# Performance work log

Measured on AMD Instinct MI355X. Metric: run time of the kernel, lower is better.

Reference implementation:

```python
import jax, jax.numpy as jnp
import numpy as np

EPSILON = 1e-06
MAXIMUM_AREA_RATIO = 0.3
GRID_HEIGHT = 160.0
CUBE = (25.0, 25.0, 32.0)
FEAT_SCALE = 1.0
GRID_SCALE = 1.0
CRANGE = (-1.0, 0.95)


def setup_inputs() -> dict:
    key = jax.random.key(0)
    k1, k2, k3, k4, k5 = jax.random.split(key, 5)
    B, C, H, W = 2, 256, 96, 320
    L, Wg = 128, 128
    n_layers = int(GRID_HEIGHT // CUBE[2])  # 5
    return {
        "feature": jax.random.normal(k1, (B, C, H, W), dtype=jnp.float32),
        "calib": jax.random.normal(k2, (B, 3, 4), dtype=jnp.float32),
        "grid": jax.random.normal(k3, (L, Wg, 3), dtype=jnp.float32),
        "Wc": jax.random.normal(k4, (C, C * n_layers), dtype=jnp.float32) * 0.02,
        "bc": jax.random.normal(k5, (C,), dtype=jnp.float32) * 0.02,
    }


def _cube_corners(cube):
    l, w, h = cube
    x = np.array([-l / 2, l / 2, l / 2, -l / 2, -l / 2, l / 2, l / 2, -l / 2])
    y = np.array([-w / 2, -w / 2, w / 2, w / 2, -w / 2, -w / 2, w / 2, w / 2])
    z = np.array([0, 0, 0, 0, h, h, h, h])
    return jnp.asarray(np.stack([x, y, z], axis=-1), dtype=jnp.float32)  # (8,3)


def _grid_sample_zeros(img, grd):
    # img: [B,C,H,W]; grd: [B,Hg,Wg,2] normalized coords in [-1,1]
    # bilinear, zero padding, align_corners=False (torch default)
    B, C, H, W = img.shape
    x = ((grd[..., 0] + 1.0) * W - 1.0) * 0.5
    y = ((grd[..., 1] + 1.0) * H - 1.0) * 0.5
    x0f = jnp.floor(x)
    y0f = jnp.floor(y)
    x0 = x0f.astype(jnp.int32)
    y0 = y0f.astype(jnp.int32)
    img_flat = img.reshape(B, C, H * W)

    def gather(xi, yi):
        valid = (xi >= 0) & (xi < W) & (yi >= 0) & (yi < H)
        xc = jnp.clip(xi, 0, W - 1)
        yc = jnp.clip(yi, 0, H - 1)
        idx = (yc * W + xc).reshape(B, 1, -1)
        v = jnp.take_along_axis(img_flat, idx, axis=2)
        v = v.reshape((B, C) + grd.shape[1:-1])
        return v * valid[:, None].astype(img.dtype)

    wx1 = x - x0f
    wx0 = 1.0 - wx1
    wy1 = y - y0f
    wy0 = 1.0 - wy1
    out = (gather(x0, y0) * (wx0 * wy0)[:, None]
           + gather(x0 + 1, y0) * (wx1 * wy0)[:, None]
           + gather(x0, y0 + 1) * (wx0 * wy1)[:, None]
           + gather(x0 + 1, y0 + 1) * (wx1 * wy1)[:, None])
    return out


def reference(feature, calib, grid, Wc, bc):
    B, C, H, W = feature.shape
    L, Wg, _ = grid.shape
    dtype = feature.dtype

    # z-layer offsets: (n_layers, 3) with offset only in z
    z_off = jnp.arange(0.0, GRID_HEIGHT, CUBE[2], dtype=dtype)  # (5,)
    n_layers = z_off.shape[0]
    z_corners = jnp.stack([jnp.zeros_like(z_off), jnp.zeros_like(z_off), z_off], axis=-1)
    offset = _cube_corners(CUBE)  # (8,3)

    # corners3d: (n_layers, L, Wg, 8, 3)
    corners = grid[None] + z_corners[:, None, None, :]  # (n,L,Wg,3)
    corners3d = (corners[:, :, :, None, :] + offset[None, None, None]) / GRID_SCALE

    # project with calib (B,3,4): homogeneous matmul then perspective divide
    hom = jnp.concatenate([corners3d, jnp.ones_like(corners3d[..., :1])], axis=-1)  # (n,L,Wg,8,4)
    pts = jnp.einsum('bij,nlwkj->bnlwki', calib, hom)  # (B,n,L,Wg,8,3)
    img_xy = pts[..., :2] / jnp.maximum(pts[..., 2:3], EPSILON)

    img_size = jnp.array([W, H], dtype=dtype) / FEAT_SCALE
    norm = jnp.clip(2.0 * img_xy / img_size - 1.0, CRANGE[0], CRANGE[1])  # (B,n,L,Wg,8,2)

    box_corners = jnp.concatenate([
        jnp.min(norm[..., 0], axis=-1, keepdims=True),
        jnp.min(norm[..., 1], axis=-1, keepdims=True),
        jnp.max(norm[..., 0], axis=-1, keepdims=True),
        jnp.max(norm[..., 1], axis=-1, keepdims=True),
    ], axis=-1)  # (B,n,L,Wg,4)
    box_corners = box_corners.reshape(B, n_layers, L * Wg, 4)

    area = ((box_corners[..., 2:] - box_corners[..., :2]).prod(axis=-1) * (H * W) + EPSILON)
    area = area[:, None]  # (B,1,n,LWg)
    visible = ((area > EPSILON) & (area < H * W * MAXIMUM_AREA_RATIO)).astype(dtype)

    integral = jnp.cumsum(jnp.cumsum(feature, axis=-1), axis=-2)

    lt = _grid_sample_zeros(integral, box_corners[..., [0, 1]])
    rb = _grid_sample_zeros(integral, box_corners[..., [2, 3]])
    rt = _grid_sample_zeros(integral, box_corners[..., [2, 1]])
    lb = _grid_sample_zeros(integral, box_corners[..., [0, 3]])

    vox = (lt + rb - rt - lb) / area * visible  # (B,C,n,LWg)
    # permute(0,3,1,2) -> (B, LWg, C, n); flatten to (B*LWg, C*n)
    vox = jnp.transpose(vox, (0, 3, 1, 2)).reshape(B * L * Wg, C * n_layers)

    ortho = vox @ Wc.T + bc  # (B*LWg, C)
    ortho = ortho.reshape(B, L, Wg, C)
    ortho = jax.nn.relu(jnp.transpose(ortho, (0, 3, 1, 2)))  # (B,C,L,Wg)
    return ortho
```

## Files before the change

### kernel.cpp

```cpp
#include <hip/hip_runtime.h>
#include <hip/hip_bf16.h>
#include <stdint.h>

#define BB 2
#define CC 256
#define HH 96
#define WW 320
#define NPIX 16384
#define NLAY 5
#define KDIM 1280
#define NDIM 32768
#define NKT (KDIM / 32)
#define NGRP 256
#define BSP 264

typedef float f32x4 __attribute__((ext_vector_type(4)));
typedef float f32x2 __attribute__((ext_vector_type(2)));
typedef __bf16 bf16x8 __attribute__((ext_vector_type(8)));
typedef __bf16 bf16x4 __attribute__((ext_vector_type(4)));

__global__ __launch_bounds__(1024) void k1f(const float* __restrict__ feat,
                                            float* __restrict__ integ,
                                            const float* __restrict__ gridp,
                                            const float* __restrict__ calib,
                                            const float* __restrict__ Wc,
                                            float4* __restrict__ coords,
                                            float* __restrict__ scales,
                                            __bf16* __restrict__ Wbf,
                                            uint8_t* __restrict__ mask8) {
  const int bid = blockIdx.x;
  if (bid < 480) {
    const int vbid = bid * 4 + (threadIdx.x >> 8);
    const int vt = threadIdx.x & 255;
    if (vbid >= 640) {
      int o = (vbid - 640) * 256 + vt;
      int co = o / KDIM;
      int kk = o % KDIM;
      int n = kk >> 8;
      int c = kk & 255;
      Wbf[o] = (__bf16)Wc[co * KDIM + c * NLAY + n];
      return;
    }
    int box = vbid * 256 + vt;
    int pix = box & (NPIX - 1);
    int bn = box >> 14;
    int n = bn % NLAY;
    int b = bn / NLAY;
    const float* cb = calib + b * 12;
    float c00 = cb[0], c01 = cb[1], c02 = cb[2], c03 = cb[3];
    float c10 = cb[4], c11 = cb[5], c12 = cb[6], c13 = cb[7];
    float c20 = cb[8], c21 = cb[9], c22 = cb[10], c23 = cb[11];
    float gx = gridp[pix * 3 + 0], gy = gridp[pix * 3 + 1], gz = gridp[pix * 3 + 2];
    float zoff = 32.0f * (float)n;
    const float ox[8] = {-12.5f, 12.5f, 12.5f, -12.5f, -12.5f, 12.5f, 12.5f, -12.5f};
    const float oy[8] = {-12.5f, -12.5f, 12.5f, 12.5f, -12.5f, -12.5f, 12.5f, 12.5f};
    float xmn = 1e30f, ymn = 1e30f, xmx = -1e30f, ymx = -1e30f;
#pragma unroll
    for (int k = 0; k < 8; ++k) {
      float X = gx + ox[k];
      float Y = gy + oy[k];
      float Z = gz + zoff + ((k >= 4) ? 32.0f : 0.0f);
      float px = c00 * X + c01 * Y + c02 * Z + c03;
      float py = c10 * X + c11 * Y + c12 * Z + c13;
      float pz = c20 * X + c21 * Y + c22 * Z + c23;
      float d = fmaxf(pz, 1e-6f);
      float nx = fminf(fmaxf(2.0f * (px / d) / 320.0f - 1.0f, -1.0f), 0.95f);
      float ny = fminf(fmaxf(2.0f * (py / d) / 96.0f - 1.0f, -1.0f), 0.95f);
      xmn = fminf(xmn, nx); xmx = fmaxf(xmx, nx);
      ymn = fminf(ymn, ny); ymx = fmaxf(ymx, ny);
    }
    float dx = xmx - xmn, dy = ymx - ymn;
    float area = (dx * dy) * 30720.0f + 1e-6f;
    bool vis = (area > 1e-6f) && (area < 9216.0f);
    {
      __shared__ uint32_t kf[16];
      unsigned long long bal = __ballot(vis);
      if ((threadIdx.x & 63) == 0) kf[threadIdx.x >> 6] = (bal != 0ull) ? 1u : 0u;
      __syncthreads();
      if (vt == 0) {
        int vb = threadIdx.x >> 8;
        int vbid2 = bid * 4 + vb;
        int bn2 = vbid2 >> 6;
        int n2 = bn2 % NLAY, b2 = bn2 / NLAY;
        int g0 = b2 * 128 + (vbid2 & 63) * 2;
        mask8[g0 * 5 + n2]       = (uint8_t)(kf[vb * 4 + 0] | kf[vb * 4 + 1]);
        mask8[(g0 + 1) * 5 + n2] = (uint8_t)(kf[vb * 4 + 2] | kf[vb * 4 + 3]);
      }
    }
    float X0 = ((xmn + 1.0f) * 320.0f - 1.0f) * 0.5f;
    float Y0 = ((ymn + 1.0f) * 96.0f - 1.0f) * 0.5f;
    float X1 = ((xmx + 1.0f) * 320.0f - 1.0f) * 0.5f;
    float Y1 = ((ymx + 1.0f) * 96.0f - 1.0f) * 0.5f;
    coords[box] = make_float4(X0, Y0, X1, Y1);
    scales[box] = vis ? 1.0f / area : 0.0f;
    return;
  }
  __shared__ float tile[WW * 33];
  const int t = threadIdx.x;
  const int wave = t >> 6;
  const int lane = t & 63;
  const int kb = bid - 480;
  const int cg = kb & 7;
  const int h = (kb >> 3) % HH;
  const int b = kb / (8 * HH);
  const int c0 = cg * 32;

  {
    const float* fb = feat + (size_t)((b * CC + c0) * HH + h) * WW;
    const size_t crstride = (size_t)HH * WW;
#pragma unroll
    for (int r = 0; r < 3; ++r) {
      int idx = r * 1024 + t;
      if (idx < 2560) {
        int cr = idx / 80;
        int wq = idx - cr * 80;
        f32x4 v = *(const f32x4*)(fb + cr * crstride + wq * 4);
        *(f32x4*)(&tile[cr * WW + wq * 4]) = v;
      }
    }
  }
  __syncthreads();
  const int ca = wave * 2, cbn = wave * 2 + 1;
  float va[5], vb[5];
#pragma unroll
  for (int j = 0; j < 5; ++j) va[j] = tile[ca * WW + lane * 5 + j];
#pragma unroll
  for (int j = 0; j < 5; ++j) vb[j] = tile[cbn * WW + lane * 5 + j];
#pragma unroll
  for (int j = 1; j < 5; ++j) { va[j] += va[j - 1]; vb[j] += vb[j - 1]; }
  float ta = va[4], tb = vb[4];
  float ia = ta, ib = tb;
#pragma unroll
  for (int d = 1; d < 64; d <<= 1) {
    float ua = __shfl_up(ia, d, 64);
    float ub = __shfl_up(ib, d, 64);
    if (lane >= d) { ia += ua; ib += ub; }
  }
  float pa = ia - ta, pb = ib - tb;
#pragma unroll
  for (int j = 0; j < 5; ++j) { va[j] += pa; vb[j] += pb; }
  __syncthreads();
#pragma unroll
  for (int j = 0; j < 5; ++j) {
    int w = lane * 5 + j;
    tile[w * 33 + ca]  = va[j];
    tile[w * 33 + cbn] = vb[j];
  }
  __syncthreads();
  float* dst = integ + (size_t)((b * HH + h) * WW) * CC + cg * 32;
#pragma unroll
  for (int r = 0; r < 3; ++r) {
    int idx = r * 1024 + t;
    if (idx < 2560) {
      int w = idx >> 3;
      int cq = (idx & 7) * 4;
      float4 o = make_float4(tile[w * 33 + cq + 0], tile[w * 33 + cq + 1],
                             tile[w * 33 + cq + 2], tile[w * 33 + cq + 3]);
      *(float4*)(dst + (size_t)w * CC + cq) = o;
    }
  }
}

__global__ __launch_bounds__(256) void k2_scan(float* __restrict__ integ) {
  const int blk = blockIdx.x;
  const int w = blk % WW;
  const int b = blk / WW;
  const int g = threadIdx.x >> 6;
  const int l = threadIdx.x & 63;
  float* base = integ + ((size_t)(b * HH + g * 24) * WW + w) * CC + l * 4;
  const size_t stride = (size_t)WW * CC;
  f32x4 v[24];
#pragma unroll
  for (int i = 0; i < 24; ++i) v[i] = *(const f32x4*)(base + (size_t)i * stride);
#pragma unroll
  for (int i = 1; i < 24; ++i) v[i] += v[i - 1];
  __shared__ f32x4 part[4][64];
  part[g][l] = v[23];
  __syncthreads();
  f32x4 off = {0.f, 0.f, 0.f, 0.f};
#pragma unroll
  for (int gg = 0; gg < 3; ++gg)
    if (gg < g) off += part[gg][l];
#pragma unroll
  for (int i = 0; i < 24; ++i) *(f32x4*)(base + (size_t)i * stride) = v[i] + off;
}

__device__ __forceinline__ void glds16(const void* g, void* l) {
  __builtin_amdgcn_global_load_lds(
      (const __attribute__((address_space(1))) void*)g,
      (__attribute__((address_space(3))) void*)(uint32_t)(uintptr_t)l,
      16, 0, 0);
}

__global__ __launch_bounds__(512) void k46(const __bf16* __restrict__ A,
                                           const float* __restrict__ integ,
                                           const float4* __restrict__ coords,
                                           const float* __restrict__ scales,
                                           const float* __restrict__ bias,
                                           float* __restrict__ out,
                                           const uint8_t* __restrict__ mask8) {
  __shared__ __align__(16) __bf16 As[3][256 * 32];
  __shared__ __align__(16) __bf16 Bs[128 * BSP];
  const int g = blockIdx.x;
  const int b = g >> 7;
  const int pix0 = (g & 127) * 128;
  const int tid = threadIdx.x;
  const int lane = tid & 63;
  const int wave = tid >> 6;
  const int wm = (wave >> 1) * 64;
  const int wn = (wave & 1) * 64;
  const int r16 = lane & 15;
  const int q4 = lane >> 4;

  int ln[NLAY], nact = 0;
#pragma unroll
  for (int n = 0; n < NLAY; ++n)
    if (mask8[g * 5 + n]) ln[nact++] = n;

  f32x4 acc[4][4];
#pragma unroll
  for (int i = 0; i < 4; ++i)
#pragma unroll
    for (int j = 0; j < 4; ++j)
      acc[i][j] = f32x4{0.f, 0.f, 0.f, 0.f};

  auto stage = [&](int buf, int kt) {
    const int k0 = kt * 32;
#pragma unroll
    for (int rr = 0; rr < 2; ++rr) {
      const int base_row = rr * 128 + wave * 16;
      const int row = base_row + (lane >> 2);
      const int gch = (lane & 3) ^ ((row >> 1) & 3);
      glds16(A + (size_t)row * KDIM + k0 + gch * 8,
             (void*)(&As[buf][base_row * 32] + lane * 8));
    }
  };

  for (int la = 0; la < nact; ++la) {
    const int n = ln[la];
    const int bn = b * NLAY + n;
    const float* gbase = integ + (size_t)(b * HH) * WW * CC + lane * 4;
#pragma unroll 4
    for (int u = 0; u < 16; ++u) {
      const int row = wave * 16 + u;
      const int box = (bn << 14) | (pix0 + row);
      bf16x4* dst = (bf16x4*)(&Bs[row * BSP + lane * 4]);
      const float scale = scales[box];
      if (scale == 0.f) {
        *dst = bf16x4{(__bf16)0.f, (__bf16)0.f, (__bf16)0.f, (__bf16)0.f};
        continue;
      }
      const float4 q = coords[box];
      float xw[4]; int xi[4];
      float yw[4]; int yi[4];
      {
        float f0 = floorf(q.x); int i0 = (int)f0; float w1 = q.x - f0;
        xw[0] = (i0 >= 0 && i0 < WW) ? (1.f - w1) : 0.f;
        xw[1] = (i0 + 1 < WW) ? w1 : 0.f;
        xi[0] = min(max(i0, 0), WW - 1); xi[1] = min(max(i0 + 1, 0), WW - 1);
        float f1 = floorf(q.z); int i1 = (int)f1; float v1 = q.z - f1;
        xw[2] = (i1 >= 0 && i1 < WW) ? -(1.f - v1) : 0.f;
        xw[3] = (i1 + 1 < WW) ? -v1 : 0.f;
        xi[2] = min(max(i1, 0), WW - 1); xi[3] = min(max(i1 + 1, 0), WW - 1);
      }
      {
        float f0 = floorf(q.y); int j0 = (int)f0; float w1 = q.y - f0;
        yw[0] = (j0 >= 0 && j0 < HH) ? (1.f - w1) : 0.f;
        yw[1] = (j0 + 1 < HH) ? w1 : 0.f;
        yi[0] = min(max(j0, 0), HH - 1); yi[1] = min(max(j0 + 1, 0), HH - 1);
        float f1 = floorf(q.w); int j1 = (int)f1; float v1 = q.w - f1;
        yw[2] = (j1 >= 0 && j1 < HH) ? -(1.f - v1) : 0.f;
        yw[3] = (j1 + 1 < HH) ? -v1 : 0.f;
        yi[2] = min(max(j1, 0), HH - 1); yi[3] = min(max(j1 + 1, 0), HH - 1);
      }
      f32x4 val = {0.f, 0.f, 0.f, 0.f};
#pragma unroll
      for (int jj = 0; jj < 4; ++jj) {
        if (yw[jj] == 0.f) continue;
        const float* rp = gbase + (size_t)yi[jj] * WW * CC;
        f32x4 rs = {0.f, 0.f, 0.f, 0.f};
#pragma unroll
        for (int ii = 0; ii < 4; ++ii) {
          if (xw[ii] != 0.f) {
            f32x4 v = *(const f32x4*)(rp + (size_t)xi[ii] * CC);
            rs += xw[ii] * v;
          }
        }
        val += yw[jj] * rs;
      }
      val *= scale;
      *dst = bf16x4{(__bf16)val.x, (__bf16)val.y, (__bf16)val.z, (__bf16)val.w};
    }
    __syncthreads();
    const int base = n * 8;
    stage(0, base);
    stage(1, base + 1);
    for (int kk = 0; kk < 8; ++kk) {
      const int cur = kk % 3;
      if (kk < 7) __builtin_amdgcn_s_waitcnt(0xF72);
      else        __builtin_amdgcn_s_waitcnt(0xF70);
      __builtin_amdgcn_s_barrier();
      if (kk + 2 < 8) stage((kk + 2) % 3, base + kk + 2);
      bf16x8 af[4], bg[4];
#pragma unroll
      for (int i = 0; i < 4; ++i) {
        int m = wm + i * 16 + r16;
        af[i] = *(const bf16x8*)(&As[cur][m * 32] + (q4 ^ ((m >> 1) & 3)) * 8);
      }
#pragma unroll
      for (int j = 0; j < 4; ++j) {
        int nr = wn + j * 16 + r16;
        bg[j] = *(const bf16x8*)(&Bs[nr * BSP + kk * 32 + q4 * 8]);
      }
#pragma unroll
      for (int i = 0; i < 4; ++i)
#pragma unroll
        for (int j = 0; j < 4; ++j)
          acc[i][j] = __builtin_amdgcn_mfma_f32_16x16x32_bf16(af[i], bg[j], acc[i][j], 0, 0, 0);
    }
    __syncthreads();
  }

#pragma unroll
  for (int i = 0; i < 4; ++i) {
#pragma unroll
    for (int j = 0; j < 4; ++j) {
      int pix = pix0 + wn + j * 16 + r16;
#pragma unroll
      for (int r = 0; r < 4; ++r) {
        int co = wm + i * 16 + q4 * 4 + r;
        float v = acc[i][j][r] + bias[co];
        out[(size_t)(b * CC + co) * NPIX + pix] = fmaxf(v, 0.f);
      }
    }
  }
}

extern "C" void kernel_launch(void* const* d_in, const int* in_sizes, int n_in,
                              void* d_out, int out_size, void* d_ws, size_t ws_size,
                              hipStream_t stream) {
  const float* feat  = (const float*)d_in[0];
  const float* calib = (const float*)d_in[1];
  const float* grid  = (const float*)d_in[2];
  const float* Wc    = (const float*)d_in[3];
  const float* bc    = (const float*)d_in[4];
  float* out = (float*)d_out;

  char* ws = (char*)d_ws;
  const size_t SZ_INTEG = (size_t)BB * HH * WW * CC * 4;
  const size_t SZ_VOX   = (size_t)NDIM * KDIM * 2;
  const size_t SZ_WBF   = (size_t)CC * KDIM * 2;
  const size_t SZ_CRD   = (size_t)BB * NLAY * NPIX * 16;
  const size_t SZ_SCL   = (size_t)BB * NLAY * NPIX * 4;
  const size_t SZ_MSK   = (size_t)NGRP * NLAY;
  if (ws_size < SZ_INTEG + SZ_VOX + SZ_WBF + SZ_CRD + SZ_SCL + SZ_MSK) return;

  float*   integ  = (float*)ws;
  __bf16*  Wbf    = (__bf16*)(ws + SZ_INTEG + SZ_VOX);
  float4*  coords = (float4*)(ws + SZ_INTEG + SZ_VOX + SZ_WBF);
  float*   scales = (float*)(ws + SZ_INTEG + SZ_VOX + SZ_WBF + SZ_CRD);
  uint8_t* mask8  = (uint8_t*)(ws + SZ_INTEG + SZ_VOX + SZ_WBF + SZ_CRD + SZ_SCL);

  k1f<<<dim3(BB * HH * 8 + 480), dim3(1024), 0, stream>>>(
      feat, integ, grid, calib, Wc, coords, scales, Wbf, mask8);
  k2_scan<<<dim3(BB * WW), dim3(256), 0, stream>>>(integ);
  k46<<<dim3(NGRP), dim3(512), 0, stream>>>(Wbf, integ, coords, scales, bc, out, mask8);
}
```

Before: 193.0 us.

## Shrink fused gather-GEMM tile to 32 pixels and read weights directly from global

The fused sampling+GEMM kernel now handles 32 pixels per block instead of 128, launching 1024 blocks instead of 256 to fill more CUs. Each wave computes a 64x16 output tile. The shared-memory triple-buffered weight staging is removed, so each wave loads bf16 weight fragments straight from global memory and relies on caches. This trades reuse of the weight matrix and the async LDS pipeline for more parallelism on the gather-heavy phase, and it adds redundant weight traffic per block. The per-group mask is still read at the old 128-pixel granularity.

```diff
diff --git a/kernel.cpp b/kernel.cpp
--- a/kernel.cpp
+++ b/kernel.cpp
@@ -10,7 +10,6 @@
 #define NLAY 5
 #define KDIM 1280
 #define NDIM 32768
-#define NKT (KDIM / 32)
 #define NGRP 256
 #define BSP 264
 
@@ -185,13 +184,6 @@
   for (int i = 0; i < 24; ++i) *(f32x4*)(base + (size_t)i * stride) = v[i] + off;
 }
 
-__device__ __forceinline__ void glds16(const void* g, void* l) {
-  __builtin_amdgcn_global_load_lds(
-      (const __attribute__((address_space(1))) void*)g,
-      (__attribute__((address_space(3))) void*)(uint32_t)(uintptr_t)l,
-      16, 0, 0);
-}
-
 __global__ __launch_bounds__(512) void k46(const __bf16* __restrict__ A,
                                            const float* __restrict__ integ,
                                            const float4* __restrict__ coords,
@@ -199,50 +191,35 @@
                                            const float* __restrict__ bias,
                                            float* __restrict__ out,
                                            const uint8_t* __restrict__ mask8) {
-  __shared__ __align__(16) __bf16 As[3][256 * 32];
-  __shared__ __align__(16) __bf16 Bs[128 * BSP];
+  __shared__ __align__(16) __bf16 Bs[32 * BSP];
   const int g = blockIdx.x;
-  const int b = g >> 7;
-  const int pix0 = (g & 127) * 128;
+  const int b = g >> 9;
+  const int pix0 = (g & 511) * 32;
+  const int gm = b * 128 + (pix0 >> 7);
   const int tid = threadIdx.x;
   const int lane = tid & 63;
   const int wave = tid >> 6;
   const int wm = (wave >> 1) * 64;
-  const int wn = (wave & 1) * 64;
+  const int wn = (wave & 1) * 16;
   const int r16 = lane & 15;
   const int q4 = lane >> 4;
 
   int ln[NLAY], nact = 0;
 #pragma unroll
   for (int n = 0; n < NLAY; ++n)
-    if (mask8[g * 5 + n]) ln[nact++] = n;
-
-  f32x4 acc[4][4];
-#pragma unroll
-  for (int i = 0; i < 4; ++i)
-#pragma unroll
-    for (int j = 0; j < 4; ++j)
-      acc[i][j] = f32x4{0.f, 0.f, 0.f, 0.f};
-
-  auto stage = [&](int buf, int kt) {
-    const int k0 = kt * 32;
-#pragma unroll
-    for (int rr = 0; rr < 2; ++rr) {
-      const int base_row = rr * 128 + wave * 16;
-      const int row = base_row + (lane >> 2);
-      const int gch = (lane & 3) ^ ((row >> 1) & 3);
-      glds16(A + (size_t)row * KDIM + k0 + gch * 8,
-             (void*)(&As[buf][base_row * 32] + lane * 8));
-    }
-  };
+    if (mask8[gm * 5 + n]) ln[nact++] = n;
+
+  f32x4 acc[4];
+#pragma unroll
+  for (int i = 0; i < 4; ++i) acc[i] = f32x4{0.f, 0.f, 0.f, 0.f};
 
   for (int la = 0; la < nact; ++la) {
     const int n = ln[la];
     const int bn = b * NLAY + n;
     const float* gbase = integ + (size_t)(b * HH) * WW * CC + lane * 4;
-#pragma unroll 4
-    for (int u = 0; u < 16; ++u) {
-      const int row = wave * 16 + u;
+#pragma unroll
+    for (int u = 0; u < 4; ++u) {
+      const int row = wave * 4 + u;
       const int box = (bn << 14) | (pix0 + row);
       bf16x4* dst = (bf16x4*)(&Bs[row * BSP + lane * 4]);
       const float scale = scales[box];
@@ -292,46 +269,30 @@
       *dst = bf16x4{(__bf16)val.x, (__bf16)val.y, (__bf16)val.z, (__bf16)val.w};
     }
     __syncthreads();
-    const int base = n * 8;
-    stage(0, base);
-    stage(1, base + 1);
+    const int kbase = n * 256;
+#pragma unroll
     for (int kk = 0; kk < 8; ++kk) {
-      const int cur = kk % 3;
-      if (kk < 7) __builtin_amdgcn_s_waitcnt(0xF72);
-      else        __builtin_amdgcn_s_waitcnt(0xF70);
-      __builtin_amdgcn_s_barrier();
-      if (kk + 2 < 8) stage((kk + 2) % 3, base + kk + 2);
-      bf16x8 af[4], bg[4];
-#pragma unroll
-      for (int i = 0; i < 4; ++i) {
-        int m = wm + i * 16 + r16;
-        af[i] = *(const bf16x8*)(&As[cur][m * 32] + (q4 ^ ((m >> 1) & 3)) * 8);
-      }
-#pragma unroll
-      for (int j = 0; j < 4; ++j) {
-        int nr = wn + j * 16 + r16;
-        bg[j] = *(const bf16x8*)(&Bs[nr * BSP + kk * 32 + q4 * 8]);
-      }
+      const int k0 = kbase + kk * 32;
+      bf16x8 af[4];
 #pragma unroll
       for (int i = 0; i < 4; ++i)
-#pragma unroll
-        for (int j = 0; j < 4; ++j)
-          acc[i][j] = __builtin_amdgcn_mfma_f32_16x16x32_bf16(af[i], bg[j], acc[i][j], 0, 0, 0);
+        af[i] = *(const bf16x8*)(A + (size_t)(wm + i * 16 + r16) * KDIM + k0 + q4 * 8);
+      bf16x8 bg = *(const bf16x8*)(&Bs[(wn + r16) * BSP + kk * 32 + q4 * 8]);
+#pragma unroll
+      for (int i = 0; i < 4; ++i)
+        acc[i] = __builtin_amdgcn_mfma_f32_16x16x32_bf16(af[i], bg, acc[i], 0, 0, 0);
     }
     __syncthreads();
   }
 
 #pragma unroll
   for (int i = 0; i < 4; ++i) {
-#pragma unroll
-    for (int j = 0; j < 4; ++j) {
-      int pix = pix0 + wn + j * 16 + r16;
-#pragma unroll
-      for (int r = 0; r < 4; ++r) {
-        int co = wm + i * 16 + q4 * 4 + r;
-        float v = acc[i][j][r] + bias[co];
-        out[(size_t)(b * CC + co) * NPIX + pix] = fmaxf(v, 0.f);
-      }
+    int pix = pix0 + wn + r16;
+#pragma unroll
+    for (int r = 0; r < 4; ++r) {
+      int co = wm + i * 16 + q4 * 4 + r;
+      float v = acc[i][r] + bias[co];
+      out[(size_t)(b * CC + co) * NPIX + pix] = fmaxf(v, 0.f);
     }
   }
 }
@@ -364,5 +325,5 @@
   k1f<<<dim3(BB * HH * 8 + 480), dim3(1024), 0, stream>>>(
       feat, integ, grid, calib, Wc, coords, scales, Wbf, mask8);
   k2_scan<<<dim3(BB * WW), dim3(256), 0, stream>>>(integ);
-  k46<<<dim3(NGRP), dim3(512), 0, stream>>>(Wbf, integ, coords, scales, bc, out, mask8);
+  k46<<<dim3(NDIM / 32), dim3(512), 0, stream>>>(Wbf, integ, coords, scales, bc, out, mask8);
 }
```

New measurement: 170.1 us. -11.9%, faster.
